# Performance work log

Hardware: AMD Instinct MI355X
Metric: run time of the kernel (lower is better)

Reference implementation:

```python
import jax, jax.numpy as jnp
import numpy as np

D_MODEL = 256
N_LAYERS = 2
EXPAND = 2
D_INNER = EXPAND * D_MODEL  # 512
D_STATE = 16
D_CONV = 4
DT_RANK = max(1, D_MODEL // 16)  # 16


def _selective_scan(x, dt, B, C, A, D):
    # x, dt: [b, l, d]   B, C: [b, l, n]   A: [d, n]   D: [d]
    dA = jnp.exp(jnp.einsum('bld,dn->bldn', dt, A))          # discretized state matrix
    dBx = jnp.einsum('bld,bln,bld->bldn', dt, B, x)           # dt * B * u

    def step(h, inp):
        dA_t, dBx_t, C_t = inp                                 # [b,d,n],[b,d,n],[b,n]
        h = dA_t * h + dBx_t
        y = jnp.einsum('bdn,bn->bd', h, C_t)
        return h, y

    h0 = jnp.zeros((x.shape[0], A.shape[0], A.shape[1]), x.dtype)
    _, ys = jax.lax.scan(step, h0, (jnp.moveaxis(dA, 1, 0),
                                    jnp.moveaxis(dBx, 1, 0),
                                    jnp.moveaxis(C, 1, 0)))
    return jnp.moveaxis(ys, 0, 1) + x * D                      # [b, l, d]


def _mamba_block(z, in_w, conv_w, conv_b, xp_w, dt_w, dt_b, A_log, Dp, out_w):
    b, l, _ = z.shape
    xz = z @ in_w.T                                            # [b, l, 2*d_inner]
    x, gate = jnp.split(xz, 2, axis=-1)
    # causal depthwise conv1d over time
    xt = jnp.transpose(x, (0, 2, 1))                            # [b, d_inner, l]
    xt = jax.lax.conv_general_dilated(
        xt, conv_w[:, None, :], window_strides=(1,),
        padding=[(D_CONV - 1, 0)], feature_group_count=D_INNER)
    x = jax.nn.silu(jnp.transpose(xt, (0, 2, 1)) + conv_b)      # [b, l, d_inner]
    x_dbl = x @ xp_w.T                                          # [b, l, dt_rank + 2*d_state]
    dt, Bm, Cm = jnp.split(x_dbl, [DT_RANK, DT_RANK + D_STATE], axis=-1)
    dt = jax.nn.softplus(dt @ dt_w.T + dt_b)                    # [b, l, d_inner]
    A = -jnp.exp(A_log)                                         # [d_inner, d_state]
    y = _selective_scan(x, dt, Bm, Cm, A, Dp)
    y = y * jax.nn.silu(gate)
    return y @ out_w.T                                          # [b, l, d_model]


def setup_inputs() -> dict:
    key = jax.random.key(0)
    ks = jax.random.split(key, 9)
    B, L = 2, 4096
    z = jax.random.normal(ks[0], (B, L, D_MODEL), jnp.float32)
    s = 0.02
    in_proj_w = jax.random.normal(ks[1], (N_LAYERS, 2 * D_INNER, D_MODEL), jnp.float32) * s
    conv_w = jax.random.normal(ks[2], (N_LAYERS, D_INNER, D_CONV), jnp.float32) * 0.2
    conv_b = jnp.zeros((N_LAYERS, D_INNER), jnp.float32)
    x_proj_w = jax.random.normal(ks[3], (N_LAYERS, DT_RANK + 2 * D_STATE, D_INNER), jnp.float32) * s
    dt_proj_w = jax.random.normal(ks[4], (N_LAYERS, D_INNER, DT_RANK), jnp.float32) * 0.1
    dt_proj_b = jax.random.uniform(ks[5], (N_LAYERS, D_INNER), jnp.float32, -4.0, -2.0)
    A_log = jnp.log(jnp.broadcast_to(jnp.arange(1, D_STATE + 1, dtype=jnp.float32),
                                     (N_LAYERS, D_INNER, D_STATE)))
    D_param = jnp.ones((N_LAYERS, D_INNER), jnp.float32)
    out_proj_w = jax.random.normal(ks[6], (N_LAYERS, D_MODEL, D_INNER), jnp.float32) * s
    return {"z": z, "in_proj_w": in_proj_w, "conv_w": conv_w, "conv_b": conv_b,
            "x_proj_w": x_proj_w, "dt_proj_w": dt_proj_w, "dt_proj_b": dt_proj_b,
            "A_log": A_log, "D_param": D_param, "out_proj_w": out_proj_w}


def reference(z, in_proj_w, conv_w, conv_b, x_proj_w, dt_proj_w, dt_proj_b,
              A_log, D_param, out_proj_w):
    for i in range(N_LAYERS):
        z = _mamba_block(z, in_proj_w[i], conv_w[i], conv_b[i], x_proj_w[i],
                         dt_proj_w[i], dt_proj_b[i], A_log[i], D_param[i], out_proj_w[i])
    return z
```

## Files before the change

### kernel.cpp

```cpp
#include <hip/hip_runtime.h>
#include <hip/hip_bf16.h>
#include <cstdint>
#include <cstddef>

#define DM   256
#define DI   512
#define DS   16
#define LSEQ 4096
#define BATCH 2
#define BLROWS (BATCH * LSEQ)
#define NCH  128
#define CLEN 32
#define XCP  520

typedef __bf16 bf16x8 __attribute__((ext_vector_type(8)));
typedef float  f32x4  __attribute__((ext_vector_type(4)));
typedef unsigned short u16;
typedef u16 u16x8 __attribute__((ext_vector_type(8)));
typedef u16 u16x4 __attribute__((ext_vector_type(4)));

__device__ __forceinline__ u16 f2bfu(float f) {
    union { float f; unsigned u; } c; c.f = f;
    unsigned u = c.u;
    return (u16)((u + 0x7fffu + ((u >> 16) & 1u)) >> 16);
}
__device__ __forceinline__ float bfu2f(u16 u) {
    union { unsigned u; float f; } c; c.u = ((unsigned)u) << 16; return c.f;
}
__device__ __forceinline__ float siluf(float v) {
    return v * (1.0f / (1.0f + __expf(-v)));
}
__device__ __forceinline__ void gload_lds16(const void* g, void* l) {
    __builtin_amdgcn_global_load_lds(
        (const __attribute__((address_space(1))) unsigned int*)g,
        (__attribute__((address_space(3))) unsigned int*)l, 16, 0, 0);
}

#define N_INW  (2*1024*256)
#define N_OUTW (2*256*512)
#define N_XPW  (2*64*512)
#define N_Z    (BLROWS*DM)
__global__ __launch_bounds__(256) void cast_all_k(
    const float* __restrict__ in_w, const float* __restrict__ out_w,
    const float* __restrict__ xp_w, const float* __restrict__ z,
    u16* __restrict__ inw_bf, u16* __restrict__ outw_bf,
    u16* __restrict__ xpw_bf, u16* __restrict__ z_bf) {
    int i = blockIdx.x * 256 + threadIdx.x;
    if (i < N_INW) {
        inw_bf[i] = f2bfu(in_w[i]);
    } else if (i < N_INW + N_OUTW) {
        int j = i - N_INW;
        outw_bf[j] = f2bfu(out_w[j]);
    } else if (i < N_INW + N_OUTW + N_XPW) {
        int j = i - (N_INW + N_OUTW);
        int k = j & 511, o = (j >> 9) & 63, l = j >> 15;
        xpw_bf[j] = f2bfu((o < 48) ? xp_w[(l * 48 + o) * 512 + k] : 0.0f);
    } else {
        int j = i - (N_INW + N_OUTW + N_XPW);
        z_bf[j] = f2bfu(z[j]);
    }
}

__global__ __launch_bounds__(256) void gemm_in_k(
    const __bf16* __restrict__ A, const __bf16* __restrict__ B,
    u16* __restrict__ Cb, int M, int N, int K) {
    __shared__ __bf16 As[128 * 32];
    __shared__ __bf16 Bs[128 * 32];
    int tid = threadIdx.x, wave = tid >> 6, lane = tid & 63;
    int bm = blockIdx.x * 128, bn = blockIdx.y * 128;
    int wm = (wave & 1) * 64, wn = (wave >> 1) * 64;
    int row = lane & 15, q = lane >> 4;
    int srow = lane >> 2, sseg = lane & 3;
    f32x4 acc[4][4] = {};
    for (int k0 = 0; k0 < K; k0 += 32) {
        #pragma unroll
        for (int i = 0; i < 2; ++i) {
            int r0 = wave * 32 + i * 16;
            gload_lds16(A + (size_t)(bm + r0 + srow) * K + k0 + sseg * 8, As + r0 * 32);
            gload_lds16(B + (size_t)(bn + r0 + srow) * K + k0 + sseg * 8, Bs + r0 * 32);
        }
        __syncthreads();
        bf16x8 af[4], bfr[4];
        #pragma unroll
        for (int mi = 0; mi < 4; ++mi)
            af[mi] = *(const bf16x8*)&As[(wm + mi*16 + row) * 32 + q * 8];
        #pragma unroll
        for (int ni = 0; ni < 4; ++ni)
            bfr[ni] = *(const bf16x8*)&Bs[(wn + ni*16 + row) * 32 + q * 8];
        #pragma unroll
        for (int mi = 0; mi < 4; ++mi)
            #pragma unroll
            for (int ni = 0; ni < 4; ++ni)
                acc[mi][ni] = __builtin_amdgcn_mfma_f32_16x16x32_bf16(
                    af[mi], bfr[ni], acc[mi][ni], 0, 0, 0);
        __syncthreads();
    }
    #pragma unroll
    for (int mi = 0; mi < 4; ++mi)
        #pragma unroll
        for (int r = 0; r < 4; ++r) {
            size_t gr = (size_t)(bm + wm + mi*16 + q*4 + r) * N;
            #pragma unroll
            for (int ni = 0; ni < 4; ++ni)
                Cb[gr + bn + wn + ni*16 + row] = f2bfu(acc[mi][ni][r]);
        }
}

__global__ __launch_bounds__(512) void fused_a_k(
    const u16* __restrict__ xz, const float* __restrict__ cw,
    const float* __restrict__ cb, const __bf16* __restrict__ xpw,
    const float* __restrict__ dtw, const float* __restrict__ dtb,
    const float* __restrict__ Alog,
    u16* __restrict__ xcb, u16* __restrict__ dtob,
    float* __restrict__ BCg, u16* __restrict__ Pb, u16* __restrict__ Sb) {
    __shared__ u16 xc_s[CLEN * XCP];
    __shared__ float xd_s[CLEN * 68];
    int tid = threadIdx.x;
    int c = blockIdx.x, b = blockIdx.y;
    int bl0 = b * LSEQ + c * CLEN;
    int d = tid;

    {
        float w0 = cw[d*4], w1 = cw[d*4+1], w2 = cw[d*4+2], w3 = cw[d*4+3];
        float bias = cb[d];
        float xm3 = 0.f, xm2 = 0.f, xm1 = 0.f;
        int l0 = c * CLEN;
        if (l0 - 3 >= 0) xm3 = bfu2f(xz[(size_t)(bl0 - 3) * 1024 + d]);
        if (l0 - 2 >= 0) xm2 = bfu2f(xz[(size_t)(bl0 - 2) * 1024 + d]);
        if (l0 - 1 >= 0) xm1 = bfu2f(xz[(size_t)(bl0 - 1) * 1024 + d]);
        #pragma unroll 4
        for (int t = 0; t < CLEN; ++t) {
            float xcur = bfu2f(xz[(size_t)(bl0 + t) * 1024 + d]);
            float acc = fmaf(w0, xm3, fmaf(w1, xm2, fmaf(w2, xm1, fmaf(w3, xcur, bias))));
            float v = siluf(acc);
            u16 vb = f2bfu(v);
            xc_s[t * XCP + d] = vb;
            xcb[(size_t)(bl0 + t) * DI + d] = vb;
            xm3 = xm2; xm2 = xm1; xm1 = xcur;
        }
    }
    __syncthreads();

    {
        int wave = tid >> 6, lane = tid & 63;
        int row = lane & 15, q = lane >> 4;
        int mt = wave & 1, nt = wave >> 2;
        nt = wave >> 1;
        f32x4 acc = {0.f, 0.f, 0.f, 0.f};
        #pragma unroll
        for (int kb = 0; kb < 16; ++kb) {
            bf16x8 a = *(const bf16x8*)&xc_s[(mt*16 + row) * XCP + kb*32 + q*8];
            bf16x8 bb = *(const bf16x8*)(xpw + (size_t)(nt*16 + row) * 512 + kb*32 + q*8);
            acc = __builtin_amdgcn_mfma_f32_16x16x32_bf16(a, bb, acc, 0, 0, 0);
        }
        #pragma unroll
        for (int r = 0; r < 4; ++r)
            xd_s[(mt*16 + q*4 + r) * 68 + nt*16 + row] = acc[r];
    }
    __syncthreads();

    for (int i = tid; i < CLEN * 32; i += 512) {
        int t = i >> 5, cc = i & 31;
        BCg[((size_t)(b*NCH + c) * CLEN + t) * 32 + cc] = xd_s[t*68 + 16 + cc];
    }

    {
        float dtwr[16];
        const f32x4* w4 = (const f32x4*)(dtw + (size_t)d * 16);
        #pragma unroll
        for (int g = 0; g < 4; ++g) { f32x4 v = w4[g];
            dtwr[g*4] = v[0]; dtwr[g*4+1] = v[1]; dtwr[g*4+2] = v[2]; dtwr[g*4+3] = v[3]; }
        float dtbv = dtb[d];
        float Ac[16];
        const f32x4* a4 = (const f32x4*)(Alog + (size_t)d * 16);
        #pragma unroll
        for (int g = 0; g < 4; ++g) { f32x4 v = a4[g];
            #pragma unroll
            for (int j = 0; j < 4; ++j) Ac[g*4+j] = -__expf(v[j]); }
        bool fastp = true;
        #pragma unroll
        for (int n = 1; n < 16; ++n)
            fastp = fastp && (fabsf(Ac[n] - (float)(n+1) * Ac[0])
                              <= 1e-4f * fabsf(Ac[n]));
        float p[16], s[16];
        #pragma unroll
        for (int n = 0; n < 16; ++n) { p[n] = 1.0f; s[n] = 0.0f; }
        for (int t = 0; t < CLEN; ++t) {
            float acc = dtbv;
            #pragma unroll
            for (int r = 0; r < 16; ++r) acc = fmaf(xd_s[t*68 + r], dtwr[r], acc);
            float dtv = (acc > 20.0f) ? acc : logf(1.0f + __expf(acc));
            dtob[(size_t)(bl0 + t) * DI + d] = f2bfu(dtv);
            float xv = bfu2f(xc_s[t * XCP + d]);
            float dx = dtv * xv;
            float an[16];
            if (fastp) {
                float a0 = __expf(dtv * Ac[0]);
                an[0] = a0;
                #pragma unroll
                for (int n = 1; n < 16; ++n) an[n] = an[n-1] * a0;
            } else {
                #pragma unroll
                for (int n = 0; n < 16; ++n) an[n] = __expf(dtv * Ac[n]);
            }
            #pragma unroll
            for (int n = 0; n < 16; ++n) {
                s[n] = fmaf(an[n], s[n], xd_s[t*68 + 16 + n] * dx);
                p[n] *= an[n];
            }
        }
        size_t base = ((size_t)(b*NCH + c) * DI + d) * 16;
        u16x8 pv0, pv1, sv0, sv1;
        #pragma unroll
        for (int n = 0; n < 8; ++n) {
            pv0[n] = f2bfu(p[n]);   pv1[n] = f2bfu(p[8+n]);
            sv0[n] = f2bfu(s[n]);   sv1[n] = f2bfu(s[8+n]);
        }
        *(u16x8*)(Pb + base)     = pv0;  *(u16x8*)(Pb + base + 8) = pv1;
        *(u16x8*)(Sb + base)     = sv0;  *(u16x8*)(Sb + base + 8) = sv1;
    }
}

__global__ __launch_bounds__(256) void scanB_k(
    const u16* __restrict__ Pb, const u16* __restrict__ Sb,
    float* __restrict__ H) {
    int i = blockIdx.x * 256 + threadIdx.x;
    int b = i >> 11, j4 = i & 2047;
    f32x4 h = {0.f, 0.f, 0.f, 0.f};
    for (int c = 0; c < NCH; ++c) {
        size_t i4 = (size_t)(b*NCH + c) * 2048 + j4;
        u16x4 pv = ((const u16x4*)Pb)[i4];
        u16x4 sv = ((const u16x4*)Sb)[i4];
        ((f32x4*)H)[i4] = h;
        #pragma unroll
        for (int j = 0; j < 4; ++j) h[j] = fmaf(bfu2f(pv[j]), h[j], bfu2f(sv[j]));
    }
}

__global__ __launch_bounds__(512) void fused_c_k(
    const u16* __restrict__ xcb, const u16* __restrict__ dtob,
    const float* __restrict__ BCg, const float* __restrict__ H,
    const float* __restrict__ Alog, const float* __restrict__ Dp,
    const u16* __restrict__ xz, const __bf16* __restrict__ outw,
    u16* __restrict__ Ob, float* __restrict__ Of) {
    __shared__ u16 y_s[CLEN * XCP];
    __shared__ float BCs[CLEN * 32];
    int tid = threadIdx.x;
    int c = blockIdx.x, b = blockIdx.y;
    int bl0 = b * LSEQ + c * CLEN;
    int d = tid;

    for (int i = tid; i < CLEN * 32; i += 512)
        BCs[i] = BCg[(size_t)(b*NCH + c) * (CLEN*32) + i];

    float Ac[16], h[16];
    {
        const f32x4* a4 = (const f32x4*)(Alog + (size_t)d * 16);
        const f32x4* h4 = (const f32x4*)(H + ((size_t)(b*NCH + c) * DI + d) * 16);
        #pragma unroll
        for (int g = 0; g < 4; ++g) {
            f32x4 av = a4[g]; f32x4 hv = h4[g];
            #pragma unroll
            for (int j = 0; j < 4; ++j) { Ac[g*4+j] = -__expf(av[j]); h[g*4+j] = hv[j]; }
        }
    }
    bool fastp = true;
    #pragma unroll
    for (int n = 1; n < 16; ++n)
        fastp = fastp && (fabsf(Ac[n] - (float)(n+1) * Ac[0]) <= 1e-4f * fabsf(Ac[n]));
    float Dv = Dp[d];
    __syncthreads();

    #pragma unroll 4
    for (int t = 0; t < CLEN; ++t) {
        float dtv = bfu2f(dtob[(size_t)(bl0 + t) * DI + d]);
        float xv  = bfu2f(xcb[(size_t)(bl0 + t) * DI + d]);
        float gv  = bfu2f(xz[(size_t)(bl0 + t) * 1024 + DI + d]);
        float dx = dtv * xv;
        float an[16];
        if (fastp) {
            float a0 = __expf(dtv * Ac[0]);
            an[0] = a0;
            #pragma unroll
            for (int n = 1; n < 16; ++n) an[n] = an[n-1] * a0;
        } else {
            #pragma unroll
            for (int n = 0; n < 16; ++n) an[n] = __expf(dtv * Ac[n]);
        }
        float y = 0.f;
        #pragma unroll
        for (int n = 0; n < 16; ++n) {
            h[n] = fmaf(an[n], h[n], BCs[t*32 + n] * dx);
            y = fmaf(h[n], BCs[t*32 + 16 + n], y);
        }
        float yv = fmaf(xv, Dv, y) * siluf(gv);
        y_s[t * XCP + d] = f2bfu(yv);
    }
    __syncthreads();

    {
        int wave = tid >> 6, lane = tid & 63;
        int row = lane & 15, q = lane >> 4;
        int mt = wave & 1, ng = wave >> 1;
        f32x4 acc[4] = {};
        #pragma unroll
        for (int kb = 0; kb < 16; ++kb) {
            bf16x8 a = *(const bf16x8*)&y_s[(mt*16 + row) * XCP + kb*32 + q*8];
            #pragma unroll
            for (int ni = 0; ni < 4; ++ni) {
                bf16x8 bb = *(const bf16x8*)(outw +
                    (size_t)(ng*64 + ni*16 + row) * 512 + kb*32 + q*8);
                acc[ni] = __builtin_amdgcn_mfma_f32_16x16x32_bf16(a, bb, acc[ni], 0, 0, 0);
            }
        }
        #pragma unroll
        for (int r = 0; r < 4; ++r) {
            size_t gr = (size_t)(bl0 + mt*16 + q*4 + r) * DM;
            #pragma unroll
            for (int ni = 0; ni < 4; ++ni) {
                int gc = ng*64 + ni*16 + row;
                if (Ob) Ob[gr + gc] = f2bfu(acc[ni][r]);
                else    Of[gr + gc] = acc[ni][r];
            }
        }
    }
}

extern "C" void kernel_launch(void* const* d_in, const int* in_sizes, int n_in,
                              void* d_out, int out_size, void* d_ws, size_t ws_size,
                              hipStream_t stream) {
    (void)in_sizes; (void)n_in; (void)out_size; (void)ws_size;
    const float* z_in   = (const float*)d_in[0];
    const float* in_w   = (const float*)d_in[1];
    const float* conv_w = (const float*)d_in[2];
    const float* conv_b = (const float*)d_in[3];
    const float* xp_w   = (const float*)d_in[4];
    const float* dt_w   = (const float*)d_in[5];
    const float* dt_b   = (const float*)d_in[6];
    const float* A_log  = (const float*)d_in[7];
    const float* D_par  = (const float*)d_in[8];
    const float* out_w  = (const float*)d_in[9];
    float* outp = (float*)d_out;

    char* p = (char*)d_ws;
    auto alloc = [&](size_t bytes) { char* r = p; p += (bytes + 255) & ~(size_t)255; return r; };
    u16* z_bf    = (u16*)alloc((size_t)BLROWS*DM*2);
    u16* z2_bf   = (u16*)alloc((size_t)BLROWS*DM*2);
    u16* xz_bf   = (u16*)alloc((size_t)BLROWS*1024*2);
    u16* xc_bf   = (u16*)alloc((size_t)BLROWS*DI*2);
    u16* dt_bf   = (u16*)alloc((size_t)BLROWS*DI*2);
    u16* inw_bf  = (u16*)alloc((size_t)2*1024*256*2);
    u16* outw_bf = (u16*)alloc((size_t)2*256*512*2);
    u16* xpw_bf  = (u16*)alloc((size_t)2*64*512*2);
    float* BCg   = (float*)alloc((size_t)BATCH*NCH*CLEN*32*4);
    u16* Pbuf    = (u16*)alloc((size_t)BATCH*NCH*DI*DS*2);
    u16* Sbuf    = (u16*)alloc((size_t)BATCH*NCH*DI*DS*2);
    float* Hbuf  = (float*)alloc((size_t)BATCH*NCH*DI*DS*4);

    cast_all_k<<<(N_INW + N_OUTW + N_XPW + N_Z)/256, 256, 0, stream>>>(
        in_w, out_w, xp_w, z_in, inw_bf, outw_bf, xpw_bf, z_bf);

    const u16* zcur = z_bf;
    for (int l = 0; l < 2; ++l) {
        gemm_in_k<<<dim3(BLROWS/128, 1024/128), 256, 0, stream>>>(
            (const __bf16*)zcur, (const __bf16*)(inw_bf + (size_t)l*1024*256),
            xz_bf, BLROWS, 1024, 256);
        fused_a_k<<<dim3(NCH, BATCH), 512, 0, stream>>>(
            xz_bf, conv_w + (size_t)l*DI*4, conv_b + (size_t)l*DI,
            (const __bf16*)(xpw_bf + (size_t)l*64*512),
            dt_w + (size_t)l*DI*16, dt_b + (size_t)l*DI,
            A_log + (size_t)l*DI*DS,
            xc_bf, dt_bf, BCg, Pbuf, Sbuf);
        scanB_k<<<16, 256, 0, stream>>>(Pbuf, Sbuf, Hbuf);
        fused_c_k<<<dim3(NCH, BATCH), 512, 0, stream>>>(
            xc_bf, dt_bf, BCg, Hbuf,
            A_log + (size_t)l*DI*DS, D_par + (size_t)l*DI,
            xz_bf, (const __bf16*)(outw_bf + (size_t)l*256*512),
            (l == 0) ? z2_bf : nullptr, (l == 1) ? outp : nullptr);
        zcur = z2_bf;
    }
}
```

Baseline: 255.1 us.

## Fuse input projection GEMM into chunk kernel, computing conv halo rows locally

```diff
diff --git a/kernel.cpp b/kernel.cpp
--- a/kernel.cpp
+++ b/kernel.cpp
@@ -12,6 +12,13 @@
 #define NCH  128
 #define CLEN 32
 #define XCP  520
+
+#define OFF_INW 0
+#define OFF_XC  0
+#define OFF_Z   65536
+#define OFF_XD  65536
+#define OFF_XX  90880
+#define SMEM_SZ 127280
 
 typedef __bf16 bf16x8 __attribute__((ext_vector_type(8)));
 typedef float  f32x4  __attribute__((ext_vector_type(4)));
@@ -61,78 +68,89 @@
     }
 }
 
-__global__ __launch_bounds__(256) void gemm_in_k(
-    const __bf16* __restrict__ A, const __bf16* __restrict__ B,
-    u16* __restrict__ Cb, int M, int N, int K) {
-    __shared__ __bf16 As[128 * 32];
-    __shared__ __bf16 Bs[128 * 32];
-    int tid = threadIdx.x, wave = tid >> 6, lane = tid & 63;
-    int bm = blockIdx.x * 128, bn = blockIdx.y * 128;
-    int wm = (wave & 1) * 64, wn = (wave >> 1) * 64;
-    int row = lane & 15, q = lane >> 4;
-    int srow = lane >> 2, sseg = lane & 3;
-    f32x4 acc[4][4] = {};
-    for (int k0 = 0; k0 < K; k0 += 32) {
-        #pragma unroll
-        for (int i = 0; i < 2; ++i) {
-            int r0 = wave * 32 + i * 16;
-            gload_lds16(A + (size_t)(bm + r0 + srow) * K + k0 + sseg * 8, As + r0 * 32);
-            gload_lds16(B + (size_t)(bn + r0 + srow) * K + k0 + sseg * 8, Bs + r0 * 32);
-        }
-        __syncthreads();
-        bf16x8 af[4], bfr[4];
-        #pragma unroll
-        for (int mi = 0; mi < 4; ++mi)
-            af[mi] = *(const bf16x8*)&As[(wm + mi*16 + row) * 32 + q * 8];
-        #pragma unroll
-        for (int ni = 0; ni < 4; ++ni)
-            bfr[ni] = *(const bf16x8*)&Bs[(wn + ni*16 + row) * 32 + q * 8];
-        #pragma unroll
-        for (int mi = 0; mi < 4; ++mi)
-            #pragma unroll
-            for (int ni = 0; ni < 4; ++ni)
-                acc[mi][ni] = __builtin_amdgcn_mfma_f32_16x16x32_bf16(
-                    af[mi], bfr[ni], acc[mi][ni], 0, 0, 0);
-        __syncthreads();
-    }
-    #pragma unroll
-    for (int mi = 0; mi < 4; ++mi)
-        #pragma unroll
-        for (int r = 0; r < 4; ++r) {
-            size_t gr = (size_t)(bm + wm + mi*16 + q*4 + r) * N;
-            #pragma unroll
-            for (int ni = 0; ni < 4; ++ni)
-                Cb[gr + bn + wn + ni*16 + row] = f2bfu(acc[mi][ni][r]);
-        }
-}
-
 __global__ __launch_bounds__(512) void fused_a_k(
-    const u16* __restrict__ xz, const float* __restrict__ cw,
-    const float* __restrict__ cb, const __bf16* __restrict__ xpw,
+    const u16* __restrict__ zin, const u16* __restrict__ inw,
+    const float* __restrict__ cw, const float* __restrict__ cb,
+    const __bf16* __restrict__ xpw,
     const float* __restrict__ dtw, const float* __restrict__ dtb,
     const float* __restrict__ Alog,
-    u16* __restrict__ xcb, u16* __restrict__ dtob,
+    u16* __restrict__ xcb, u16* __restrict__ dtob, u16* __restrict__ gateb,
     float* __restrict__ BCg, u16* __restrict__ Pb, u16* __restrict__ Sb) {
-    __shared__ u16 xc_s[CLEN * XCP];
-    __shared__ float xd_s[CLEN * 68];
+    __shared__ __align__(16) char smem[SMEM_SZ];
+    u16*  inw_s = (u16*)(smem + OFF_INW);
+    u16*  z_s   = (u16*)(smem + OFF_Z);
+    u16*  xx_s  = (u16*)(smem + OFF_XX);
+    u16*  xc_s  = (u16*)(smem + OFF_XC);
+    float* xd_s = (float*)(smem + OFF_XD);
     int tid = threadIdx.x;
     int c = blockIdx.x, b = blockIdx.y;
     int bl0 = b * LSEQ + c * CLEN;
+    int wave = tid >> 6, lane = tid & 63;
+    int row = lane & 15, q = lane >> 4;
     int d = tid;
+
+    for (int idx = tid; idx < 48 * 32; idx += 512) {
+        int r = idx >> 5, c8 = idx & 31;
+        u16x8 v = {0,0,0,0,0,0,0,0};
+        if (r < 35 && (c > 0 || r >= 3))
+            v = *(const u16x8*)(zin + (size_t)(bl0 - 3 + r) * DM + c8 * 8);
+        *(u16x8*)(z_s + r * 264 + c8 * 8) = v;
+    }
+    __syncthreads();
+
+    for (int g = 0; g < 8; ++g) {
+        {
+            int pos = lane & 31, roff = lane >> 5;
+            #pragma unroll
+            for (int i = 0; i < 8; ++i) {
+                int r_abs = wave * 16 + i * 2 + roff;
+                int chunk = (pos - r_abs) & 31;
+                gload_lds16(inw + (size_t)(g * 128 + r_abs) * 256 + chunk * 8,
+                            inw_s + (wave * 16 + i * 2) * 256);
+            }
+        }
+        __syncthreads();
+        f32x4 acc[3] = {};
+        #pragma unroll
+        for (int kb = 0; kb < 8; ++kb) {
+            int cidx = kb * 4 + q;
+            int r_abs = wave * 16 + row;
+            int pos = (cidx + r_abs) & 31;
+            bf16x8 bb = *(const bf16x8*)(inw_s + r_abs * 256 + pos * 8);
+            #pragma unroll
+            for (int mt = 0; mt < 3; ++mt) {
+                bf16x8 a = *(const bf16x8*)(z_s + (mt*16 + row) * 264 + kb*32 + q*8);
+                acc[mt] = __builtin_amdgcn_mfma_f32_16x16x32_bf16(a, bb, acc[mt], 0, 0, 0);
+            }
+        }
+        __syncthreads();
+        int col = g * 128 + wave * 16 + row;
+        #pragma unroll
+        for (int mt = 0; mt < 3; ++mt)
+            #pragma unroll
+            for (int r = 0; r < 4; ++r) {
+                int grow = mt * 16 + q * 4 + r;
+                if (g < 4) {
+                    if (grow < 35) xx_s[grow * XCP + col] = f2bfu(acc[mt][r]);
+                } else {
+                    int t = grow - 3;
+                    if (t >= 0 && t < CLEN)
+                        gateb[(size_t)(bl0 + t) * DI + (col - 512)] = f2bfu(acc[mt][r]);
+                }
+            }
+    }
+    __syncthreads();
 
     {
         float w0 = cw[d*4], w1 = cw[d*4+1], w2 = cw[d*4+2], w3 = cw[d*4+3];
         float bias = cb[d];
-        float xm3 = 0.f, xm2 = 0.f, xm1 = 0.f;
-        int l0 = c * CLEN;
-        if (l0 - 3 >= 0) xm3 = bfu2f(xz[(size_t)(bl0 - 3) * 1024 + d]);
-        if (l0 - 2 >= 0) xm2 = bfu2f(xz[(size_t)(bl0 - 2) * 1024 + d]);
-        if (l0 - 1 >= 0) xm1 = bfu2f(xz[(size_t)(bl0 - 1) * 1024 + d]);
+        float xm3 = bfu2f(xx_s[0*XCP + d]);
+        float xm2 = bfu2f(xx_s[1*XCP + d]);
+        float xm1 = bfu2f(xx_s[2*XCP + d]);
         #pragma unroll 4
         for (int t = 0; t < CLEN; ++t) {
-            float xcur = bfu2f(xz[(size_t)(bl0 + t) * 1024 + d]);
-            float acc = fmaf(w0, xm3, fmaf(w1, xm2, fmaf(w2, xm1, fmaf(w3, xcur, bias))));
-            float v = siluf(acc);
+            float xcur = bfu2f(xx_s[(t + 3) * XCP + d]);
+            float v = siluf(fmaf(w0, xm3, fmaf(w1, xm2, fmaf(w2, xm1, fmaf(w3, xcur, bias)))));
             u16 vb = f2bfu(v);
             xc_s[t * XCP + d] = vb;
             xcb[(size_t)(bl0 + t) * DI + d] = vb;
@@ -142,10 +160,7 @@
     __syncthreads();
 
     {
-        int wave = tid >> 6, lane = tid & 63;
-        int row = lane & 15, q = lane >> 4;
-        int mt = wave & 1, nt = wave >> 2;
-        nt = wave >> 1;
+        int mt = wave & 1, nt = wave >> 1;
         f32x4 acc = {0.f, 0.f, 0.f, 0.f};
         #pragma unroll
         for (int kb = 0; kb < 16; ++kb) {
@@ -180,8 +195,7 @@
         bool fastp = true;
         #pragma unroll
         for (int n = 1; n < 16; ++n)
-            fastp = fastp && (fabsf(Ac[n] - (float)(n+1) * Ac[0])
-                              <= 1e-4f * fabsf(Ac[n]));
+            fastp = fastp && (fabsf(Ac[n] - (float)(n+1) * Ac[0]) <= 1e-4f * fabsf(Ac[n]));
         float p[16], s[16];
         #pragma unroll
         for (int n = 0; n < 16; ++n) { p[n] = 1.0f; s[n] = 0.0f; }
@@ -241,7 +255,7 @@
     const u16* __restrict__ xcb, const u16* __restrict__ dtob,
     const float* __restrict__ BCg, const float* __restrict__ H,
     const float* __restrict__ Alog, const float* __restrict__ Dp,
-    const u16* __restrict__ xz, const __bf16* __restrict__ outw,
+    const u16* __restrict__ gateb, const __bf16* __restrict__ outw,
     u16* __restrict__ Ob, float* __restrict__ Of) {
     __shared__ u16 y_s[CLEN * XCP];
     __shared__ float BCs[CLEN * 32];
@@ -275,7 +289,7 @@
     for (int t = 0; t < CLEN; ++t) {
         float dtv = bfu2f(dtob[(size_t)(bl0 + t) * DI + d]);
         float xv  = bfu2f(xcb[(size_t)(bl0 + t) * DI + d]);
-        float gv  = bfu2f(xz[(size_t)(bl0 + t) * 1024 + DI + d]);
+        float gv  = bfu2f(gateb[(size_t)(bl0 + t) * DI + d]);
         float dx = dtv * xv;
         float an[16];
         if (fastp) {
@@ -346,9 +360,9 @@
     auto alloc = [&](size_t bytes) { char* r = p; p += (bytes + 255) & ~(size_t)255; return r; };
     u16* z_bf    = (u16*)alloc((size_t)BLROWS*DM*2);
     u16* z2_bf   = (u16*)alloc((size_t)BLROWS*DM*2);
-    u16* xz_bf   = (u16*)alloc((size_t)BLROWS*1024*2);
     u16* xc_bf   = (u16*)alloc((size_t)BLROWS*DI*2);
     u16* dt_bf   = (u16*)alloc((size_t)BLROWS*DI*2);
+    u16* gate_bf = (u16*)alloc((size_t)BLROWS*DI*2);
     u16* inw_bf  = (u16*)alloc((size_t)2*1024*256*2);
     u16* outw_bf = (u16*)alloc((size_t)2*256*512*2);
     u16* xpw_bf  = (u16*)alloc((size_t)2*64*512*2);
@@ -362,20 +376,18 @@
 
     const u16* zcur = z_bf;
     for (int l = 0; l < 2; ++l) {
-        gemm_in_k<<<dim3(BLROWS/128, 1024/128), 256, 0, stream>>>(
-            (const __bf16*)zcur, (const __bf16*)(inw_bf + (size_t)l*1024*256),
-            xz_bf, BLROWS, 1024, 256);
         fused_a_k<<<dim3(NCH, BATCH), 512, 0, stream>>>(
-            xz_bf, conv_w + (size_t)l*DI*4, conv_b + (size_t)l*DI,
+            zcur, inw_bf + (size_t)l*1024*256,
+            conv_w + (size_t)l*DI*4, conv_b + (size_t)l*DI,
             (const __bf16*)(xpw_bf + (size_t)l*64*512),
             dt_w + (size_t)l*DI*16, dt_b + (size_t)l*DI,
             A_log + (size_t)l*DI*DS,
-            xc_bf, dt_bf, BCg, Pbuf, Sbuf);
+            xc_bf, dt_bf, gate_bf, BCg, Pbuf, Sbuf);
         scanB_k<<<16, 256, 0, stream>>>(Pbuf, Sbuf, Hbuf);
         fused_c_k<<<dim3(NCH, BATCH), 512, 0, stream>>>(
             xc_bf, dt_bf, BCg, Hbuf,
             A_log + (size_t)l*DI*DS, D_par + (size_t)l*DI,
-            xz_bf, (const __bf16*)(outw_bf + (size_t)l*256*512),
+            gate_bf, (const __bf16*)(outw_bf + (size_t)l*256*512),
             (l == 0) ? z2_bf : nullptr, (l == 1) ? outp : nullptr);
         zcur = z2_bf;
     }
```

Result: slower. 265.2 us (+4.0%).
